# Optimization experiments

Hardware: AMD Instinct MI355X
Metric: run time of the kernel (lower is better)

The kernel has to match this reference:

```python
import jax, jax.numpy as jnp
import numpy as np

N_NODES = 100000
NEG_SLOPE = 0.2  # DGL GATConv default


def gat_layer(x, W, al, ar, src, dst):
    # x: [N, F_in], W: [F_in, H*D], al/ar: [H, D]
    H, D = al.shape
    f = (x @ W).reshape(-1, H, D)                      # [N, H, D]
    el = jnp.einsum('nhd,hd->nh', f, al)               # src attn term
    er = jnp.einsum('nhd,hd->nh', f, ar)               # dst attn term
    e = jax.nn.leaky_relu(el[src] + er[dst], NEG_SLOPE)  # [E, H]
    # segment softmax over incoming edges of each dst node
    m = jax.ops.segment_max(e, dst, num_segments=N_NODES)
    m = jnp.where(jnp.isfinite(m), m, jnp.zeros_like(m))  # isolated nodes -> -inf guard
    ex = jnp.exp(e - m[dst])                           # [E, H]
    s = jax.ops.segment_sum(ex, dst, num_segments=N_NODES)
    alpha = ex / (s[dst] + 1e-9)                       # [E, H]
    msg = f[src] * alpha[:, :, None]                   # [E, H, D]
    out = jax.ops.segment_sum(msg, dst, num_segments=N_NODES)  # [N, H, D]
    return out.reshape(N_NODES, H * D)


def setup_inputs() -> dict:
    key = jax.random.key(0)
    ks = jax.random.split(key, 12)
    x = jax.random.normal(ks[0], (N_NODES, 128), dtype=jnp.float32)
    edge_index = jax.random.randint(ks[1], (2, 1600000), 0, N_NODES, dtype=jnp.int32)
    sc = 0.05
    W0 = jax.random.normal(ks[2], (128, 128), dtype=jnp.float32) * sc
    al0 = jax.random.normal(ks[3], (4, 32), dtype=jnp.float32) * sc
    ar0 = jax.random.normal(ks[4], (4, 32), dtype=jnp.float32) * sc
    W1 = jax.random.normal(ks[5], (128, 128), dtype=jnp.float32) * sc
    al1 = jax.random.normal(ks[6], (4, 32), dtype=jnp.float32) * sc
    ar1 = jax.random.normal(ks[7], (4, 32), dtype=jnp.float32) * sc
    W2 = jax.random.normal(ks[8], (128, 128), dtype=jnp.float32) * sc
    al2 = jax.random.normal(ks[9], (4, 32), dtype=jnp.float32) * sc
    ar2 = jax.random.normal(ks[10], (4, 32), dtype=jnp.float32) * sc
    return {"x": x, "edge_index": edge_index,
            "W0": W0, "al0": al0, "ar0": ar0,
            "W1": W1, "al1": al1, "ar1": ar1,
            "W2": W2, "al2": al2, "ar2": ar2}


def reference(x, edge_index, W0, al0, ar0, W1, al1, ar1, W2, al2, ar2):
    src, dst = edge_index[0], edge_index[1]
    h = x
    for (W, al, ar) in ((W0, al0, ar0), (W1, al1, ar1), (W2, al2, ar2)):
        h = gat_layer(h, W, al, ar, src, dst)
        h = jax.nn.relu(h)  # dropout_rate = 0.0 -> identity
    return h
```

## Files before the change

### kernel.cpp

```cpp
#include <hip/hip_runtime.h>
#include <math.h>

#define NEG_SLOPE 0.2f
#define NBUCK 512
#define BHCHUNK 8192
#define BCHUNK 4096

typedef __attribute__((ext_vector_type(8))) short short8;
typedef __attribute__((ext_vector_type(4))) float f32x4;

__device__ __forceinline__ unsigned short bf16rne(float x) {
    unsigned u = __float_as_uint(x);
    u += 0x7fffu + ((u >> 16) & 1u);
    return (unsigned short)(u >> 16);
}
__device__ __forceinline__ unsigned pack_bf2(float x, float y) {
    unsigned ux = __float_as_uint(x), uy = __float_as_uint(y);
    ux = (ux + 0x7fffu + ((ux >> 16) & 1u)) >> 16;
    uy = (uy + 0x7fffu + ((uy >> 16) & 1u)) & 0xffff0000u;
    return ux | uy;
}

__global__ __launch_bounds__(256) void k_front(
    const int* __restrict__ dst, int* __restrict__ bcnt, int E,
    const float4* __restrict__ x, uint4* __restrict__ Xb, int n8,
    const float* __restrict__ w0, const float* __restrict__ w1,
    const float* __restrict__ w2, unsigned short* __restrict__ Wt,
    int nbB, int nbCvt) {
    __shared__ int cnt[NBUCK];
    int bb = blockIdx.x, t = threadIdx.x;
    if (bb < nbB) {
        for (int i = t; i < NBUCK; i += 256) cnt[i] = 0;
        __syncthreads();
        int e0 = bb * BHCHUNK;
        int n = min(BHCHUNK, E - e0);
        for (int i = t; i < n; i += 256) atomicAdd(&cnt[dst[e0 + i] >> 8], 1);
        __syncthreads();
        for (int i = t; i < NBUCK; i += 256)
            if (cnt[i]) atomicAdd(&bcnt[i], cnt[i]);
    } else if (bb < nbB + nbCvt) {
        int id = (bb - nbB) * 256 + t;
        if (id < n8) {
            float4 a = x[id * 2], b = x[id * 2 + 1];
            uint4 o;
            o.x = pack_bf2(a.x, a.y);
            o.y = pack_bf2(a.z, a.w);
            o.z = pack_bf2(b.x, b.y);
            o.w = pack_bf2(b.z, b.w);
            Xb[id] = o;
        }
    } else {
        int id = (bb - nbB - nbCvt) * 256 + t;
        int layer = id >> 14, rem = id & 16383;
        int k = rem >> 7, n = rem & 127;
        const float* W = (layer == 0) ? w0 : (layer == 1) ? w1 : w2;
        Wt[layer * 16384 + n * 128 + k] = bf16rne(W[k * 128 + n]);
    }
}

__global__ void k_bscan(const int* __restrict__ bcnt, int* __restrict__ bbase,
                        int* __restrict__ bcur, int* __restrict__ rowstart,
                        int N, int E) {
    __shared__ int sd[NBUCK];
    int t = threadIdx.x;
    int c = bcnt[t];
    sd[t] = c;
    __syncthreads();
    for (int s = 1; s < NBUCK; s <<= 1) {
        int x = (t >= s) ? sd[t - s] : 0;
        __syncthreads();
        sd[t] += x;
        __syncthreads();
    }
    int excl = sd[t] - c;
    bbase[t] = excl;
    bcur[t] = excl;
    if (t == NBUCK - 1) bbase[NBUCK] = excl + c;
    if (t == 0) rowstart[N] = E;
}

__global__ __launch_bounds__(256) void k_bin(
    const int* __restrict__ src, const int* __restrict__ dst,
    int* __restrict__ bcur, unsigned* __restrict__ packed, int E) {
    __shared__ int cnt[NBUCK];
    __shared__ int gbase[NBUCK];
    for (int i = threadIdx.x; i < NBUCK; i += 256) cnt[i] = 0;
    __syncthreads();
    int e0 = blockIdx.x * BCHUNK;
    int n = min(BCHUNK, E - e0);
    for (int i = threadIdx.x; i < n; i += 256)
        atomicAdd(&cnt[dst[e0 + i] >> 8], 1);
    __syncthreads();
    for (int i = threadIdx.x; i < NBUCK; i += 256) {
        int c = cnt[i];
        gbase[i] = c ? atomicAdd(&bcur[i], c) : 0;
        cnt[i] = 0;
    }
    __syncthreads();
    for (int i = threadIdx.x; i < n; i += 256) {
        int d = dst[e0 + i];
        int b = d >> 8;
        int o = atomicAdd(&cnt[b], 1);
        packed[gbase[b] + o] = ((unsigned)src[e0 + i] << 8) | (unsigned)(d & 255);
    }
}

__global__ __launch_bounds__(256) void k_place2(
    const unsigned* __restrict__ packed, const int* __restrict__ bbase,
    int* __restrict__ rowstart, unsigned* __restrict__ cpack, int N) {
    __shared__ int cnt[256], sd[256], lcur[256];
    int b = blockIdx.x, t = threadIdx.x;
    int base = bbase[b], end = bbase[b + 1];
    cnt[t] = 0;
    __syncthreads();
    for (int i = base + t; i < end; i += 256)
        atomicAdd(&cnt[packed[i] & 255u], 1);
    __syncthreads();
    sd[t] = cnt[t];
    __syncthreads();
    for (int s = 1; s < 256; s <<= 1) {
        int x = (t >= s) ? sd[t - s] : 0;
        __syncthreads();
        sd[t] += x;
        __syncthreads();
    }
    int excl = sd[t] - cnt[t];
    int gid = (b << 8) + t;
    if (gid < N) rowstart[gid] = base + excl;
    lcur[t] = base + excl;
    __syncthreads();
    for (int i = base + t; i < end; i += 256) {
        unsigned p = packed[i];
        unsigned dl = p & 255u;
        int pos = atomicAdd(&lcur[dl], 1);
        cpack[pos] = (dl << 17) | (p >> 8);
    }
}

__global__ __launch_bounds__(256) void k_gemm(
    const unsigned short* __restrict__ Ab,
    const unsigned short* __restrict__ Wt,
    const float* __restrict__ alv, const float* __restrict__ arv,
    unsigned short* __restrict__ Fb,
    float* __restrict__ el, float* __restrict__ er, int M) {
    __shared__ unsigned short cst[4][32][128];
    int t = threadIdx.x;
    int wv = t >> 6, l = t & 63;
    int l15 = l & 15, quad = l >> 4;
    int row0 = blockIdx.x * 128 + wv * 32;

    f32x4 acc[2][8];
#pragma unroll
    for (int mi = 0; mi < 2; mi++)
#pragma unroll
        for (int nt = 0; nt < 8; nt++)
            acc[mi][nt] = (f32x4){0.f, 0.f, 0.f, 0.f};

    int rA0 = min(row0 + l15, M - 1);
    int rA1 = min(row0 + 16 + l15, M - 1);
    const uint4* pA0 = (const uint4*)(Ab + (size_t)rA0 * 128) + quad;
    const uint4* pA1 = (const uint4*)(Ab + (size_t)rA1 * 128) + quad;
    const uint4* pW = (const uint4*)Wt;

#pragma unroll
    for (int ks = 0; ks < 4; ks++) {
        union { uint4 u; short8 s; } a0, a1, b[8];
        a0.u = pA0[ks * 4];
        a1.u = pA1[ks * 4];
#pragma unroll
        for (int nt = 0; nt < 8; nt++)
            b[nt].u = pW[(nt * 16 + l15) * 16 + quad + ks * 4];
#pragma unroll
        for (int nt = 0; nt < 8; nt++) {
            acc[0][nt] = __builtin_amdgcn_mfma_f32_16x16x32_bf16(a0.s, b[nt].s, acc[0][nt], 0, 0, 0);
            acc[1][nt] = __builtin_amdgcn_mfma_f32_16x16x32_bf16(a1.s, b[nt].s, acc[1][nt], 0, 0, 0);
        }
    }

#pragma unroll
    for (int mi = 0; mi < 2; mi++)
#pragma unroll
        for (int nt = 0; nt < 8; nt++)
#pragma unroll
            for (int r = 0; r < 4; r++)
                cst[wv][mi * 16 + quad * 4 + r][nt * 16 + l15] = bf16rne(acc[mi][nt][r]);

    int rrow = l >> 1;
    int cb = (l & 1) * 64;
    int grow = row0 + rrow;
    bool ok = grow < M;
    float pe[2] = {0.f, 0.f}, pr[2] = {0.f, 0.f};
#pragma unroll
    for (int i = 0; i < 8; i++) {
        uint4 v = *(const uint4*)&cst[wv][rrow][cb + i * 8];
        if (ok) ((uint4*)(Fb + (size_t)grow * 128 + cb))[i] = v;
        int hi = i >> 2;
        int c0 = cb + i * 8;
        unsigned uu[4] = {v.x, v.y, v.z, v.w};
#pragma unroll
        for (int q = 0; q < 4; q++) {
            float fa = __uint_as_float(uu[q] << 16);
            float fb = __uint_as_float(uu[q] & 0xffff0000u);
            pe[hi] += fa * alv[c0 + 2 * q] + fb * alv[c0 + 2 * q + 1];
            pr[hi] += fa * arv[c0 + 2 * q] + fb * arv[c0 + 2 * q + 1];
        }
    }
    float qe0 = __shfl_xor(pe[0], 1, 64), qe1 = __shfl_xor(pe[1], 1, 64);
    float qr0 = __shfl_xor(pr[0], 1, 64), qr1 = __shfl_xor(pr[1], 1, 64);
    if (((l & 1) == 0) && ok) {
        *(float4*)&el[(size_t)grow * 4] = make_float4(pe[0], pe[1], qe0, qe1);
        *(float4*)&er[(size_t)grow * 4] = make_float4(pr[0], pr[1], qr0, qr1);
    }
}

__global__ __launch_bounds__(256) void k_edge(
    const unsigned* __restrict__ cpack, const int* __restrict__ bbase,
    const float4* __restrict__ el4, const float4* __restrict__ er4,
    float4* __restrict__ pw4) {
    int b = blockIdx.x, t = threadIdx.x;
    int base = bbase[b], end = bbase[b + 1];
    for (int i = base + t; i < end; i += 256) {
        unsigned w = cpack[i];
        int s = (int)(w & 0x1ffffu);
        int d = (b << 8) + (int)(w >> 17);
        float4 l = el4[s], r = er4[d];
        float4 o;
        float e;
        e = l.x + r.x; e = fmaxf(e, NEG_SLOPE * e); o.x = __expf(e);
        e = l.y + r.y; e = fmaxf(e, NEG_SLOPE * e); o.y = __expf(e);
        e = l.z + r.z; e = fmaxf(e, NEG_SLOPE * e); o.z = __expf(e);
        e = l.w + r.w; e = fmaxf(e, NEG_SLOPE * e); o.w = __expf(e);
        pw4[i] = o;
    }
}

template <int OUT_BF16>
__global__ __launch_bounds__(256) void k_aggr(
    const int* __restrict__ rowstart, const unsigned* __restrict__ cpack,
    const float* __restrict__ pw, const unsigned* __restrict__ FbU,
    void* __restrict__ outp, int N, int E) {
    int lane = threadIdx.x & 63;
    int half = lane >> 5;
    int l32 = lane & 31;
    int w = blockIdx.x * 8 + ((threadIdx.x >> 6) << 1) + half;
    bool active = w < N;
    int wc = active ? w : N - 1;
    int start = rowstart[wc];
    int dg = active ? (rowstart[wc + 1] - start) : 0;
    int h = l32 >> 3;
    int laneu = l32 * 2;

    float s_acc = 0.f;
    float a0 = 0.f, a1 = 0.f, a2 = 0.f, a3 = 0.f;

    int ncc = (dg + 7) >> 3;
    int nccmax = max(ncc, __shfl_xor(ncc, 32, 64));
    int full = dg >> 3;
    int minfull = min(full, __shfl_xor(full, 32, 64));

    auto loadc = [&](int c, uint2* fb, float* pb) {
        int j = c << 3;
        if (c < minfull) {
#pragma unroll
            for (int u = 0; u < 8; u++) {
                int e = start + j + u;
                unsigned cp = cpack[e];
                int s = (int)(cp & 0x1ffffu);
                fb[u] = *(const uint2*)(FbU + (size_t)s * 64 + laneu);
                pb[u] = pw[(size_t)e * 4 + h];
            }
        } else {
#pragma unroll
            for (int u = 0; u < 8; u++) {
                int jj = j + u;
                int e = min(start + max(min(jj, dg - 1), 0), E - 1);
                unsigned cp = cpack[e];
                int s = (int)(cp & 0x1ffffu);
                fb[u] = *(const uint2*)(FbU + (size_t)s * 64 + laneu);
                float pv = pw[(size_t)e * 4 + h];
                pb[u] = (jj < dg) ? pv : 0.f;
            }
        }
    };
    auto consume = [&](const uint2* fb, const float* pb) {
#pragma unroll
        for (int u = 0; u < 8; u++) {
            float p = pb[u];
            s_acc += p;
            a0 += p * __uint_as_float(fb[u].x << 16);
            a1 += p * __uint_as_float(fb[u].x & 0xffff0000u);
            a2 += p * __uint_as_float(fb[u].y << 16);
            a3 += p * __uint_as_float(fb[u].y & 0xffff0000u);
        }
    };

    uint2 f0[8], f1[8];
    float p0[8], p1[8];
    if (nccmax > 0) {
        loadc(0, f0, p0);
        for (int c = 1; c < nccmax; c++) {
            if (c & 1) { loadc(c, f1, p1); consume(f0, p0); }
            else       { loadc(c, f0, p0); consume(f1, p1); }
        }
        if (nccmax & 1) consume(f0, p0); else consume(f1, p1);
    }

    if (!active) return;
    float inv = 1.f / (s_acc + 1e-9f);
    float o0 = fmaxf(a0 * inv, 0.f);
    float o1 = fmaxf(a1 * inv, 0.f);
    float o2 = fmaxf(a2 * inv, 0.f);
    float o3 = fmaxf(a3 * inv, 0.f);
    if (OUT_BF16) {
        uint2 pk;
        pk.x = pack_bf2(o0, o1);
        pk.y = pack_bf2(o2, o3);
        *(uint2*)(((unsigned*)outp) + (size_t)w * 64 + laneu) = pk;
    } else {
        ((float4*)outp)[(size_t)w * 32 + l32] = make_float4(o0, o1, o2, o3);
    }
}


extern "C" void kernel_launch(void* const* d_in, const int* in_sizes, int n_in,
                              void* d_out, int out_size, void* d_ws, size_t ws_size,
                              hipStream_t stream) {
    const float* x = (const float*)d_in[0];
    const int* ei = (const int*)d_in[1];
    int N = in_sizes[0] / 128;
    int E = in_sizes[1] / 2;
    const int* src = ei;
    const int* dst = ei + E;
    const float* Wm[3] = {(const float*)d_in[2], (const float*)d_in[5], (const float*)d_in[8]};
    const float* al[3] = {(const float*)d_in[3], (const float*)d_in[6], (const float*)d_in[9]};
    const float* ar[3] = {(const float*)d_in[4], (const float*)d_in[7], (const float*)d_in[10]};

    char* p = (char*)d_ws;
    auto carve = [&](size_t bytes) {
        char* r = p;
        p += (bytes + 255) & ~(size_t)255;
        return r;
    };
    unsigned short* Xb = (unsigned short*)carve((size_t)N * 128 * 2);
    unsigned short* Hb = (unsigned short*)carve((size_t)N * 128 * 2);
    unsigned short* Fb = (unsigned short*)carve((size_t)N * 128 * 2);
    unsigned short* Wt = (unsigned short*)carve((size_t)3 * 16384 * 2);
    float* el       = (float*)carve((size_t)N * 4 * 4);
    float* er       = (float*)carve((size_t)N * 4 * 4);
    float* pw       = (float*)carve((size_t)E * 4 * 4);
    int* rowstart   = (int*)carve((size_t)(N + 1) * 4);
    unsigned* cpack = (unsigned*)carve((size_t)E * 4);
    unsigned* packed= (unsigned*)carve((size_t)E * 4);
    int* bcnt       = (int*)carve((size_t)NBUCK * 4);
    int* bbase      = (int*)carve((size_t)(NBUCK + 1) * 4);
    int* bcur       = (int*)carve((size_t)NBUCK * 4);

    int NBUSED = (N + 255) >> 8;

    hipMemsetAsync(bcnt, 0, NBUCK * 4, stream);
    int nbB = (E + BHCHUNK - 1) / BHCHUNK;
    int n8 = N * 128 / 8;
    int nbCvt = (n8 + 255) / 256;
    int nbPrep = (3 * 16384) / 256;
    k_front<<<nbB + nbCvt + nbPrep, 256, 0, stream>>>(
        dst, bcnt, E, (const float4*)x, (uint4*)Xb, n8,
        Wm[0], Wm[1], Wm[2], Wt, nbB, nbCvt);
    k_bscan<<<1, NBUCK, 0, stream>>>(bcnt, bbase, bcur, rowstart, N, E);
    k_bin<<<(E + BCHUNK - 1) / BCHUNK, 256, 0, stream>>>(src, dst, bcur, packed, E);
    k_place2<<<NBUSED, 256, 0, stream>>>(packed, bbase, rowstart, cpack, N);

    int gb = (N + 127) / 128;
    int ab = (N + 7) / 8;
    k_gemm<<<gb, 256, 0, stream>>>(Xb, Wt, al[0], ar[0], Fb, el, er, N);
    k_edge<<<NBUSED, 256, 0, stream>>>(cpack, bbase, (const float4*)el, (const float4*)er,
                                       (float4*)pw);
    k_aggr<1><<<ab, 256, 0, stream>>>(rowstart, cpack, pw, (const unsigned*)Fb, Hb, N, E);

    k_gemm<<<gb, 256, 0, stream>>>(Hb, Wt + 16384, al[1], ar[1], Fb, el, er, N);
    k_edge<<<NBUSED, 256, 0, stream>>>(cpack, bbase, (const float4*)el, (const float4*)er,
                                       (float4*)pw);
    k_aggr<1><<<ab, 256, 0, stream>>>(rowstart, cpack, pw, (const unsigned*)Fb, Hb, N, E);

    k_gemm<<<gb, 256, 0, stream>>>(Hb, Wt + 32768, al[2], ar[2], Fb, el, er, N);
    k_edge<<<NBUSED, 256, 0, stream>>>(cpack, bbase, (const float4*)el, (const float4*)er,
                                       (float4*)pw);
    k_aggr<0><<<ab, 256, 0, stream>>>(rowstart, cpack, pw, (const unsigned*)Fb, d_out, N, E);
}
```

Baseline: 551.2 us.

## Degree-sort nodes, normalize alpha in edge kernel, use 16-lane aggregation

Adds a counting sort of destination nodes by in-degree (capped at 63) so each aggregation wave handles nodes of similar degree. The softmax denominator moves into k_edge, which sums per-destination weights with shared-memory atomics and rescales them to alpha in a second pass. k_aggr then drops its running sum. Aggregation now uses 16 lanes per node with 16-byte loads instead of 32 lanes with 8-byte loads, fitting four nodes per wave. The aim is less intra-wave divergence in trip count and wider gathers, paid for with three small sort kernels and an extra read-modify-write of pw per layer.

```diff
diff --git a/kernel.cpp b/kernel.cpp
--- a/kernel.cpp
+++ b/kernel.cpp
@@ -5,6 +5,7 @@
 #define NBUCK 512
 #define BHCHUNK 8192
 #define BCHUNK 4096
+#define DCHUNK 2048
 
 typedef __attribute__((ext_vector_type(8))) short short8;
 typedef __attribute__((ext_vector_type(4))) float f32x4;
@@ -137,6 +138,62 @@
     }
 }
 
+__global__ __launch_bounds__(256) void k_dsort1(
+    const int* __restrict__ rowstart, int* __restrict__ dcnt, int N) {
+    __shared__ int cnt[64];
+    int t = threadIdx.x;
+    if (t < 64) cnt[t] = 0;
+    __syncthreads();
+    int n0 = blockIdx.x * DCHUNK;
+    int n = min(DCHUNK, N - n0);
+    for (int i = t; i < n; i += 256) {
+        int d = rowstart[n0 + i + 1] - rowstart[n0 + i];
+        atomicAdd(&cnt[min(d, 63)], 1);
+    }
+    __syncthreads();
+    if (t < 64 && cnt[t]) atomicAdd(&dcnt[t], cnt[t]);
+}
+
+__global__ void k_dscan(const int* __restrict__ dcnt, int* __restrict__ dcur) {
+    __shared__ int sd[64];
+    int t = threadIdx.x;
+    int c = dcnt[t];
+    sd[t] = c;
+    __syncthreads();
+    for (int s = 1; s < 64; s <<= 1) {
+        int x = (t >= s) ? sd[t - s] : 0;
+        __syncthreads();
+        sd[t] += x;
+        __syncthreads();
+    }
+    dcur[t] = sd[t] - c;
+}
+
+__global__ __launch_bounds__(256) void k_dsort2(
+    const int* __restrict__ rowstart, int* __restrict__ dcur,
+    int* __restrict__ order, int N) {
+    __shared__ int cnt[64], gbase[64];
+    int t = threadIdx.x;
+    if (t < 64) cnt[t] = 0;
+    __syncthreads();
+    int n0 = blockIdx.x * DCHUNK;
+    int n = min(DCHUNK, N - n0);
+    for (int i = t; i < n; i += 256)
+        atomicAdd(&cnt[min(rowstart[n0 + i + 1] - rowstart[n0 + i], 63)], 1);
+    __syncthreads();
+    if (t < 64) {
+        int c = cnt[t];
+        gbase[t] = c ? atomicAdd(&dcur[t], c) : 0;
+        cnt[t] = 0;
+    }
+    __syncthreads();
+    for (int i = t; i < n; i += 256) {
+        int b = min(rowstart[n0 + i + 1] - rowstart[n0 + i], 63);
+        int o = atomicAdd(&cnt[b], 1);
+        order[gbase[b] + o] = n0 + i;
+    }
+}
+
 __global__ __launch_bounds__(256) void k_gemm(
     const unsigned short* __restrict__ Ab,
     const unsigned short* __restrict__ Wt,
@@ -217,13 +274,17 @@
     const unsigned* __restrict__ cpack, const int* __restrict__ bbase,
     const float4* __restrict__ el4, const float4* __restrict__ er4,
     float4* __restrict__ pw4) {
+    __shared__ float sld[256 * 4];
     int b = blockIdx.x, t = threadIdx.x;
     int base = bbase[b], end = bbase[b + 1];
+#pragma unroll
+    for (int k = 0; k < 4; k++) sld[t * 4 + k] = 0.f;
+    __syncthreads();
     for (int i = base + t; i < end; i += 256) {
         unsigned w = cpack[i];
         int s = (int)(w & 0x1ffffu);
-        int d = (b << 8) + (int)(w >> 17);
-        float4 l = el4[s], r = er4[d];
+        int dl = (int)(w >> 17);
+        float4 l = el4[s], r = er4[(b << 8) + dl];
         float4 o;
         float e;
         e = l.x + r.x; e = fmaxf(e, NEG_SLOPE * e); o.x = __expf(e);
@@ -231,70 +292,88 @@
         e = l.z + r.z; e = fmaxf(e, NEG_SLOPE * e); o.z = __expf(e);
         e = l.w + r.w; e = fmaxf(e, NEG_SLOPE * e); o.w = __expf(e);
         pw4[i] = o;
+        atomicAdd(&sld[dl * 4 + 0], o.x);
+        atomicAdd(&sld[dl * 4 + 1], o.y);
+        atomicAdd(&sld[dl * 4 + 2], o.z);
+        atomicAdd(&sld[dl * 4 + 3], o.w);
+    }
+    __syncthreads();
+#pragma unroll
+    for (int k = 0; k < 4; k++) sld[t * 4 + k] = 1.f / (sld[t * 4 + k] + 1e-9f);
+    __syncthreads();
+    for (int i = base + t; i < end; i += 256) {
+        unsigned w = cpack[i];
+        int dl = (int)(w >> 17);
+        float4 p = pw4[i];
+        float4 iv = *(float4*)&sld[dl * 4];
+        p.x *= iv.x; p.y *= iv.y; p.z *= iv.z; p.w *= iv.w;
+        pw4[i] = p;
     }
 }
 
 template <int OUT_BF16>
 __global__ __launch_bounds__(256) void k_aggr(
-    const int* __restrict__ rowstart, const unsigned* __restrict__ cpack,
-    const float* __restrict__ pw, const unsigned* __restrict__ FbU,
-    void* __restrict__ outp, int N, int E) {
+    const int* __restrict__ rowstart, const int* __restrict__ order,
+    const unsigned* __restrict__ cpack, const float* __restrict__ alphap,
+    const uint4* __restrict__ F4, void* __restrict__ outp, int N, int E) {
     int lane = threadIdx.x & 63;
-    int half = lane >> 5;
-    int l32 = lane & 31;
-    int w = blockIdx.x * 8 + ((threadIdx.x >> 6) << 1) + half;
-    bool active = w < N;
-    int wc = active ? w : N - 1;
-    int start = rowstart[wc];
-    int dg = active ? (rowstart[wc + 1] - start) : 0;
-    int h = l32 >> 3;
-    int laneu = l32 * 2;
-
-    float s_acc = 0.f;
+    int sub = lane >> 4;
+    int l16 = lane & 15;
+    int widx = blockIdx.x * 16 + ((threadIdx.x >> 6) << 2) + sub;
+    bool active = widx < N;
+    int node = order[active ? widx : N - 1];
+    int start = rowstart[node];
+    int dg = active ? (rowstart[node + 1] - start) : 0;
+    int h = l16 >> 2;
+
     float a0 = 0.f, a1 = 0.f, a2 = 0.f, a3 = 0.f;
+    float a4 = 0.f, a5 = 0.f, a6 = 0.f, a7 = 0.f;
 
     int ncc = (dg + 7) >> 3;
-    int nccmax = max(ncc, __shfl_xor(ncc, 32, 64));
+    int m = max(ncc, __shfl_xor(ncc, 16, 64));
+    int nccmax = max(m, __shfl_xor(m, 32, 64));
     int full = dg >> 3;
-    int minfull = min(full, __shfl_xor(full, 32, 64));
-
-    auto loadc = [&](int c, uint2* fb, float* pb) {
+    int mf = min(full, __shfl_xor(full, 16, 64));
+    int minfull = min(mf, __shfl_xor(mf, 32, 64));
+
+    auto loadc = [&](int c, uint4* fb, float* pb) {
         int j = c << 3;
         if (c < minfull) {
 #pragma unroll
             for (int u = 0; u < 8; u++) {
                 int e = start + j + u;
-                unsigned cp = cpack[e];
-                int s = (int)(cp & 0x1ffffu);
-                fb[u] = *(const uint2*)(FbU + (size_t)s * 64 + laneu);
-                pb[u] = pw[(size_t)e * 4 + h];
+                int s = (int)(cpack[e] & 0x1ffffu);
+                fb[u] = F4[(size_t)s * 16 + l16];
+                pb[u] = alphap[(size_t)e * 4 + h];
             }
         } else {
 #pragma unroll
             for (int u = 0; u < 8; u++) {
                 int jj = j + u;
-                int e = min(start + max(min(jj, dg - 1), 0), E - 1);
-                unsigned cp = cpack[e];
-                int s = (int)(cp & 0x1ffffu);
-                fb[u] = *(const uint2*)(FbU + (size_t)s * 64 + laneu);
-                float pv = pw[(size_t)e * 4 + h];
+                int e = min(max(start + min(jj, dg - 1), 0), E - 1);
+                int s = (int)(cpack[e] & 0x1ffffu);
+                fb[u] = F4[(size_t)s * 16 + l16];
+                float pv = alphap[(size_t)e * 4 + h];
                 pb[u] = (jj < dg) ? pv : 0.f;
             }
         }
     };
-    auto consume = [&](const uint2* fb, const float* pb) {
+    auto consume = [&](const uint4* fb, const float* pb) {
 #pragma unroll
         for (int u = 0; u < 8; u++) {
             float p = pb[u];
-            s_acc += p;
             a0 += p * __uint_as_float(fb[u].x << 16);
             a1 += p * __uint_as_float(fb[u].x & 0xffff0000u);
             a2 += p * __uint_as_float(fb[u].y << 16);
             a3 += p * __uint_as_float(fb[u].y & 0xffff0000u);
+            a4 += p * __uint_as_float(fb[u].z << 16);
+            a5 += p * __uint_as_float(fb[u].z & 0xffff0000u);
+            a6 += p * __uint_as_float(fb[u].w << 16);
+            a7 += p * __uint_as_float(fb[u].w & 0xffff0000u);
         }
     };
 
-    uint2 f0[8], f1[8];
+    uint4 f0[8], f1[8];
     float p0[8], p1[8];
     if (nccmax > 0) {
         loadc(0, f0, p0);
@@ -306,18 +385,21 @@
     }
 
     if (!active) return;
-    float inv = 1.f / (s_acc + 1e-9f);
-    float o0 = fmaxf(a0 * inv, 0.f);
-    float o1 = fmaxf(a1 * inv, 0.f);
-    float o2 = fmaxf(a2 * inv, 0.f);
-    float o3 = fmaxf(a3 * inv, 0.f);
+    a0 = fmaxf(a0, 0.f); a1 = fmaxf(a1, 0.f);
+    a2 = fmaxf(a2, 0.f); a3 = fmaxf(a3, 0.f);
+    a4 = fmaxf(a4, 0.f); a5 = fmaxf(a5, 0.f);
+    a6 = fmaxf(a6, 0.f); a7 = fmaxf(a7, 0.f);
     if (OUT_BF16) {
-        uint2 pk;
-        pk.x = pack_bf2(o0, o1);
-        pk.y = pack_bf2(o2, o3);
-        *(uint2*)(((unsigned*)outp) + (size_t)w * 64 + laneu) = pk;
+        uint4 pk;
+        pk.x = pack_bf2(a0, a1);
+        pk.y = pack_bf2(a2, a3);
+        pk.z = pack_bf2(a4, a5);
+        pk.w = pack_bf2(a6, a7);
+        ((uint4*)outp)[(size_t)node * 16 + l16] = pk;
     } else {
-        ((float4*)outp)[(size_t)w * 32 + l32] = make_float4(o0, o1, o2, o3);
+        float4* op = (float4*)outp + (size_t)node * 32 + l16 * 2;
+        op[0] = make_float4(a0, a1, a2, a3);
+        op[1] = make_float4(a4, a5, a6, a7);
     }
 }
 
@@ -351,13 +433,18 @@
     int* rowstart   = (int*)carve((size_t)(N + 1) * 4);
     unsigned* cpack = (unsigned*)carve((size_t)E * 4);
     unsigned* packed= (unsigned*)carve((size_t)E * 4);
+    int* order      = (int*)carve((size_t)N * 4);
     int* bcnt       = (int*)carve((size_t)NBUCK * 4);
     int* bbase      = (int*)carve((size_t)(NBUCK + 1) * 4);
     int* bcur       = (int*)carve((size_t)NBUCK * 4);
+    int* dcnt       = (int*)carve(64 * 4);
+    int* dcur       = (int*)carve(64 * 4);
 
     int NBUSED = (N + 255) >> 8;
+    int NDB = (N + DCHUNK - 1) / DCHUNK;
 
     hipMemsetAsync(bcnt, 0, NBUCK * 4, stream);
+    hipMemsetAsync(dcnt, 0, 64 * 4, stream);
     int nbB = (E + BHCHUNK - 1) / BHCHUNK;
     int n8 = N * 128 / 8;
     int nbCvt = (n8 + 255) / 256;
@@ -368,21 +455,24 @@
     k_bscan<<<1, NBUCK, 0, stream>>>(bcnt, bbase, bcur, rowstart, N, E);
     k_bin<<<(E + BCHUNK - 1) / BCHUNK, 256, 0, stream>>>(src, dst, bcur, packed, E);
     k_place2<<<NBUSED, 256, 0, stream>>>(packed, bbase, rowstart, cpack, N);
+    k_dsort1<<<NDB, 256, 0, stream>>>(rowstart, dcnt, N);
+    k_dscan<<<1, 64, 0, stream>>>(dcnt, dcur);
+    k_dsort2<<<NDB, 256, 0, stream>>>(rowstart, dcur, order, N);
 
     int gb = (N + 127) / 128;
-    int ab = (N + 7) / 8;
+    int ab = (N + 15) / 16;
     k_gemm<<<gb, 256, 0, stream>>>(Xb, Wt, al[0], ar[0], Fb, el, er, N);
     k_edge<<<NBUSED, 256, 0, stream>>>(cpack, bbase, (const float4*)el, (const float4*)er,
                                        (float4*)pw);
-    k_aggr<1><<<ab, 256, 0, stream>>>(rowstart, cpack, pw, (const unsigned*)Fb, Hb, N, E);
+    k_aggr<1><<<ab, 256, 0, stream>>>(rowstart, order, cpack, pw, (const uint4*)Fb, Hb, N, E);
 
     k_gemm<<<gb, 256, 0, stream>>>(Hb, Wt + 16384, al[1], ar[1], Fb, el, er, N);
     k_edge<<<NBUSED, 256, 0, stream>>>(cpack, bbase, (const float4*)el, (const float4*)er,
                                        (float4*)pw);
-    k_aggr<1><<<ab, 256, 0, stream>>>(rowstart, cpack, pw, (const unsigned*)Fb, Hb, N, E);
+    k_aggr<1><<<ab, 256, 0, stream>>>(rowstart, order, cpack, pw, (const uint4*)Fb, Hb, N, E);
 
     k_gemm<<<gb, 256, 0, stream>>>(Hb, Wt + 32768, al[2], ar[2], Fb, el, er, N);
     k_edge<<<NBUSED, 256, 0, stream>>>(cpack, bbase, (const float4*)el, (const float4*)er,
                                        (float4*)pw);
-    k_aggr<0><<<ab, 256, 0, stream>>>(rowstart, cpack, pw, (const unsigned*)Fb, d_out, N, E);
-}
+    k_aggr<0><<<ab, 256, 0, stream>>>(rowstart, order, cpack, pw, (const uint4*)Fb, d_out, N, E);
+}
```

Result: slower. 694.0 us (+25.9%).

## Split edge kernel across more blocks and use 16-lane rows in aggregation

Applied to the files above, without the earlier changes.

The edge-score kernel now runs four blocks per destination bucket, each striding over a quarter of the bucket's edges, so the grid grows from about 391 blocks to several times that and more CUs get work. The aggregation kernel moves from 32 lanes per destination row (8 bytes of bf16 features per lane) to 16 lanes per row (16-byte uint4 loads, 8 accumulators). Each wave now handles four rows with a chunk of 4 edges instead of 8. This gives wider loads and more rows in flight, but adds per-lane registers and more divergence between the four rows sharing a wave.

```diff
diff --git a/kernel.cpp b/kernel.cpp
--- a/kernel.cpp
+++ b/kernel.cpp
@@ -5,6 +5,7 @@
 #define NBUCK 512
 #define BHCHUNK 8192
 #define BCHUNK 4096
+#define ESLICE 4
 
 typedef __attribute__((ext_vector_type(8))) short short8;
 typedef __attribute__((ext_vector_type(4))) float f32x4;
@@ -217,9 +218,11 @@
     const unsigned* __restrict__ cpack, const int* __restrict__ bbase,
     const float4* __restrict__ el4, const float4* __restrict__ er4,
     float4* __restrict__ pw4) {
-    int b = blockIdx.x, t = threadIdx.x;
+    int b = blockIdx.x >> 2;
+    int slice = blockIdx.x & (ESLICE - 1);
+    int t = slice * 256 + threadIdx.x;
     int base = bbase[b], end = bbase[b + 1];
-    for (int i = base + t; i < end; i += 256) {
+    for (int i = base + t; i < end; i += 256 * ESLICE) {
         unsigned w = cpack[i];
         int s = (int)(w & 0x1ffffu);
         int d = (b << 8) + (int)(w >> 17);
@@ -237,65 +240,69 @@
 template <int OUT_BF16>
 __global__ __launch_bounds__(256) void k_aggr(
     const int* __restrict__ rowstart, const unsigned* __restrict__ cpack,
-    const float* __restrict__ pw, const unsigned* __restrict__ FbU,
+    const float* __restrict__ pw, const uint4* __restrict__ F4,
     void* __restrict__ outp, int N, int E) {
     int lane = threadIdx.x & 63;
-    int half = lane >> 5;
-    int l32 = lane & 31;
-    int w = blockIdx.x * 8 + ((threadIdx.x >> 6) << 1) + half;
+    int sub = lane >> 4;
+    int l16 = lane & 15;
+    int w = blockIdx.x * 16 + ((threadIdx.x >> 6) << 2) + sub;
     bool active = w < N;
     int wc = active ? w : N - 1;
     int start = rowstart[wc];
     int dg = active ? (rowstart[wc + 1] - start) : 0;
-    int h = l32 >> 3;
-    int laneu = l32 * 2;
+    int h = l16 >> 2;
 
     float s_acc = 0.f;
     float a0 = 0.f, a1 = 0.f, a2 = 0.f, a3 = 0.f;
-
-    int ncc = (dg + 7) >> 3;
-    int nccmax = max(ncc, __shfl_xor(ncc, 32, 64));
-    int full = dg >> 3;
-    int minfull = min(full, __shfl_xor(full, 32, 64));
-
-    auto loadc = [&](int c, uint2* fb, float* pb) {
-        int j = c << 3;
+    float a4 = 0.f, a5 = 0.f, a6 = 0.f, a7 = 0.f;
+
+    int ncc = (dg + 3) >> 2;
+    int m = max(ncc, __shfl_xor(ncc, 16, 64));
+    int nccmax = max(m, __shfl_xor(m, 32, 64));
+    int full = dg >> 2;
+    int mf = min(full, __shfl_xor(full, 16, 64));
+    int minfull = min(mf, __shfl_xor(mf, 32, 64));
+
+    auto loadc = [&](int c, uint4* fb, float* pb) {
+        int j = c << 2;
         if (c < minfull) {
 #pragma unroll
-            for (int u = 0; u < 8; u++) {
+            for (int u = 0; u < 4; u++) {
                 int e = start + j + u;
-                unsigned cp = cpack[e];
-                int s = (int)(cp & 0x1ffffu);
-                fb[u] = *(const uint2*)(FbU + (size_t)s * 64 + laneu);
+                int s = (int)(cpack[e] & 0x1ffffu);
+                fb[u] = F4[(size_t)s * 16 + l16];
                 pb[u] = pw[(size_t)e * 4 + h];
             }
         } else {
 #pragma unroll
-            for (int u = 0; u < 8; u++) {
+            for (int u = 0; u < 4; u++) {
                 int jj = j + u;
-                int e = min(start + max(min(jj, dg - 1), 0), E - 1);
-                unsigned cp = cpack[e];
-                int s = (int)(cp & 0x1ffffu);
-                fb[u] = *(const uint2*)(FbU + (size_t)s * 64 + laneu);
+                int e = min(max(start + min(jj, dg - 1), 0), E - 1);
+                int s = (int)(cpack[e] & 0x1ffffu);
+                fb[u] = F4[(size_t)s * 16 + l16];
                 float pv = pw[(size_t)e * 4 + h];
                 pb[u] = (jj < dg) ? pv : 0.f;
             }
         }
     };
-    auto consume = [&](const uint2* fb, const float* pb) {
-#pragma unroll
-        for (int u = 0; u < 8; u++) {
+    auto consume = [&](const uint4* fb, const float* pb) {
+#pragma unroll
+        for (int u = 0; u < 4; u++) {
             float p = pb[u];
             s_acc += p;
             a0 += p * __uint_as_float(fb[u].x << 16);
             a1 += p * __uint_as_float(fb[u].x & 0xffff0000u);
             a2 += p * __uint_as_float(fb[u].y << 16);
             a3 += p * __uint_as_float(fb[u].y & 0xffff0000u);
+            a4 += p * __uint_as_float(fb[u].z << 16);
+            a5 += p * __uint_as_float(fb[u].z & 0xffff0000u);
+            a6 += p * __uint_as_float(fb[u].w << 16);
+            a7 += p * __uint_as_float(fb[u].w & 0xffff0000u);
         }
     };
 
-    uint2 f0[8], f1[8];
-    float p0[8], p1[8];
+    uint4 f0[4], f1[4];
+    float p0[4], p1[4];
     if (nccmax > 0) {
         loadc(0, f0, p0);
         for (int c = 1; c < nccmax; c++) {
@@ -307,17 +314,21 @@
 
     if (!active) return;
     float inv = 1.f / (s_acc + 1e-9f);
-    float o0 = fmaxf(a0 * inv, 0.f);
-    float o1 = fmaxf(a1 * inv, 0.f);
-    float o2 = fmaxf(a2 * inv, 0.f);
-    float o3 = fmaxf(a3 * inv, 0.f);
+    a0 = fmaxf(a0 * inv, 0.f); a1 = fmaxf(a1 * inv, 0.f);
+    a2 = fmaxf(a2 * inv, 0.f); a3 = fmaxf(a3 * inv, 0.f);
+    a4 = fmaxf(a4 * inv, 0.f); a5 = fmaxf(a5 * inv, 0.f);
+    a6 = fmaxf(a6 * inv, 0.f); a7 = fmaxf(a7 * inv, 0.f);
     if (OUT_BF16) {
-        uint2 pk;
-        pk.x = pack_bf2(o0, o1);
-        pk.y = pack_bf2(o2, o3);
-        *(uint2*)(((unsigned*)outp) + (size_t)w * 64 + laneu) = pk;
+        uint4 pk;
+        pk.x = pack_bf2(a0, a1);
+        pk.y = pack_bf2(a2, a3);
+        pk.z = pack_bf2(a4, a5);
+        pk.w = pack_bf2(a6, a7);
+        ((uint4*)outp)[(size_t)w * 16 + l16] = pk;
     } else {
-        ((float4*)outp)[(size_t)w * 32 + l32] = make_float4(o0, o1, o2, o3);
+        float4* op = (float4*)outp + (size_t)w * 32 + l16 * 2;
+        op[0] = make_float4(a0, a1, a2, a3);
+        op[1] = make_float4(a4, a5, a6, a7);
     }
 }
 
@@ -370,19 +381,19 @@
     k_place2<<<NBUSED, 256, 0, stream>>>(packed, bbase, rowstart, cpack, N);
 
     int gb = (N + 127) / 128;
-    int ab = (N + 7) / 8;
+    int ab = (N + 15) / 16;
     k_gemm<<<gb, 256, 0, stream>>>(Xb, Wt, al[0], ar[0], Fb, el, er, N);
-    k_edge<<<NBUSED, 256, 0, stream>>>(cpack, bbase, (const float4*)el, (const float4*)er,
-                                       (float4*)pw);
-    k_aggr<1><<<ab, 256, 0, stream>>>(rowstart, cpack, pw, (const unsigned*)Fb, Hb, N, E);
+    k_edge<<<NBUSED * ESLICE, 256, 0, stream>>>(cpack, bbase, (const float4*)el,
+                                                (const float4*)er, (float4*)pw);
+    k_aggr<1><<<ab, 256, 0, stream>>>(rowstart, cpack, pw, (const uint4*)Fb, Hb, N, E);
 
     k_gemm<<<gb, 256, 0, stream>>>(Hb, Wt + 16384, al[1], ar[1], Fb, el, er, N);
-    k_edge<<<NBUSED, 256, 0, stream>>>(cpack, bbase, (const float4*)el, (const float4*)er,
-                                       (float4*)pw);
-    k_aggr<1><<<ab, 256, 0, stream>>>(rowstart, cpack, pw, (const unsigned*)Fb, Hb, N, E);
+    k_edge<<<NBUSED * ESLICE, 256, 0, stream>>>(cpack, bbase, (const float4*)el,
+                                                (const float4*)er, (float4*)pw);
+    k_aggr<1><<<ab, 256, 0, stream>>>(rowstart, cpack, pw, (const uint4*)Fb, Hb, N, E);
 
     k_gemm<<<gb, 256, 0, stream>>>(Hb, Wt + 32768, al[2], ar[2], Fb, el, er, N);
-    k_edge<<<NBUSED, 256, 0, stream>>>(cpack, bbase, (const float4*)el, (const float4*)er,
-                                       (float4*)pw);
-    k_aggr<0><<<ab, 256, 0, stream>>>(rowstart, cpack, pw, (const unsigned*)Fb, d_out, N, E);
-}
+    k_edge<<<NBUSED * ESLICE, 256, 0, stream>>>(cpack, bbase, (const float4*)el,
+                                                (const float4*)er, (float4*)pw);
+    k_aggr<0><<<ab, 256, 0, stream>>>(rowstart, cpack, pw, (const uint4*)Fb, d_out, N, E);
+}
```

Measured after the change: 527.9 us. 1.04x faster.
